# Kernel optimization log

Hardware: AMD Instinct MI355X
Metric: run time of the kernel (lower is better)

## Reference

```python
import jax, jax.numpy as jnp
import numpy as np

BETA = 0.25

def setup_inputs() -> dict:
    key = jax.random.key(0)
    k1, k2 = jax.random.split(key)
    N, K, D = 32768, 8192, 512
    latents = jax.random.normal(k1, (N, D), dtype=jnp.float32)
    # torch init: uniform(-1/num_protos, 1/num_protos)
    prototypes = jax.random.uniform(k2, (K, D), dtype=jnp.float32, minval=-1.0 / K, maxval=1.0 / K)
    return {"latents": latents, "prototypes": prototypes}


def reference(latents, prototypes):
    dists = (jnp.sum(latents ** 2, axis=1, keepdims=True)
             + jnp.sum(prototypes ** 2, axis=1)
             - 2.0 * jnp.matmul(latents, prototypes.T))
    closest = jnp.argmin(dists, axis=1)  # [N]
    # one-hot @ prototypes == gather (same math, no NxK intermediate)
    quantized = prototypes[closest]  # [N, D]
    commitment_loss = jnp.mean((jax.lax.stop_gradient(quantized) - latents) ** 2)
    embedding_loss = jnp.mean((quantized - jax.lax.stop_gradient(latents)) ** 2)
    vq_loss = commitment_loss * BETA + embedding_loss
    # straight-through estimator
    quantized_st = latents + jax.lax.stop_gradient(quantized - latents)
    return quantized_st, vq_loss
```

## Files before the change

kernel.cpp:

```cpp
#include <hip/hip_runtime.h>


#define N_ROWS 32768
#define K_PROTO 8192
#define DIM 512
#define BM 128
#define BN 128
#define BKB 128
#define GROUPS 8
#define TILES 8
#define NSTEP 32
#define BUFB 16384

typedef unsigned char u8;
typedef unsigned int u32;
typedef __attribute__((ext_vector_type(4))) int i32x4;
typedef __attribute__((ext_vector_type(8))) int i32x8;
typedef __attribute__((ext_vector_type(4))) float f32x4;

__device__ __forceinline__ void async16(const void* g, void* s) {
    __builtin_amdgcn_global_load_lds(
        (const __attribute__((address_space(1))) void*)g,
        (__attribute__((address_space(3))) void*)s, 16, 0, 0);
}

__device__ __forceinline__ int pk4(float a, float b, float c, float d) {
    int v = 0;
    v = __builtin_amdgcn_cvt_pk_fp8_f32(a, b, v, false);
    v = __builtin_amdgcn_cvt_pk_fp8_f32(c, d, v, true);
    return v;
}

__global__ void __launch_bounds__(256) conv_latents(const float* __restrict__ X,
                                                    u8* __restrict__ Xf,
                                                    u32* __restrict__ best) {
    if (blockIdx.x < 128) best[blockIdx.x * 256 + threadIdx.x] = 0xFFFFFFFFu;
    size_t i = ((size_t)blockIdx.x * 256 + threadIdx.x) * 16;
    float4 a = ((const float4*)(X + i))[0];
    float4 b = ((const float4*)(X + i))[1];
    float4 c = ((const float4*)(X + i))[2];
    float4 d = ((const float4*)(X + i))[3];
    int4 o;
    o.x = pk4(a.x, a.y, a.z, a.w);
    o.y = pk4(b.x, b.y, b.z, b.w);
    o.z = pk4(c.x, c.y, c.z, c.w);
    o.w = pk4(d.x, d.y, d.z, d.w);
    *(int4*)(Xf + i) = o;
}

__global__ void __launch_bounds__(256) conv_protos(const float* __restrict__ P,
                                                   u8* __restrict__ Pf,
                                                   float* __restrict__ pnC) {
    int row  = blockIdx.x * 4 + (threadIdx.x >> 6);
    int lane = threadIdx.x & 63;
    const float* src = P + (size_t)row * DIM + lane * 8;
    float4 a = ((const float4*)src)[0];
    float4 b = ((const float4*)src)[1];
    int2 o;
    o.x = pk4(a.x * 8192.0f, a.y * 8192.0f, a.z * 8192.0f, a.w * 8192.0f);
    o.y = pk4(b.x * 8192.0f, b.y * 8192.0f, b.z * 8192.0f, b.w * 8192.0f);
    *(int2*)(Pf + (size_t)row * DIM + lane * 8) = o;
    float ss = a.x*a.x + a.y*a.y + a.z*a.z + a.w*a.w
             + b.x*b.x + b.y*b.y + b.z*b.z + b.w*b.w;
    #pragma unroll
    for (int off = 32; off; off >>= 1) ss += __shfl_down(ss, off);
    if (lane == 0) pnC[row] = ss * 8192.0f + 256.0f;
}

__device__ __forceinline__ void stage_b(const u8* __restrict__ Pf, u8* BsF,
                                        int s2, int colg, const int (&voff)[4],
                                        int tid) {
    const int t2 = s2 >> 2, kt2 = s2 & 3, sb = s2 % 3;
    const u8* src = Pf + (size_t)(colg + t2 * BN) * DIM + kt2 * BKB;
    u8* dst = BsF + sb * BUFB + tid * 16;
    #pragma unroll
    for (int i = 0; i < 4; i++)
        async16(src + voff[i], dst + i * 4096);
}

__global__ void __launch_bounds__(256, 2) vq_score_kernel(const u8* __restrict__ Xf,
                                                          const u8* __restrict__ Pf,
                                                          const float* __restrict__ pnC,
                                                          u32* __restrict__ best) {
    __shared__ __align__(16) u8 lds_raw[3 * BUFB + 4096];
    u8* BsF = lds_raw;
    const float* pcs = (const float*)(lds_raw + 3 * BUFB);

    const int tid  = threadIdx.x;
    const int row0 = blockIdx.x * BM;
    const int colg = blockIdx.y * (TILES * BN);

    const int w    = tid >> 6, lane = tid & 63;
    const int quad = lane >> 4, l15 = lane & 15;

    int voff[4];
    #pragma unroll
    for (int i = 0; i < 4; i++) {
        int f = tid + i * 256;
        int row = f >> 3, c = (f & 7) ^ (row & 7);
        voff[i] = row * DIM + c * 16;
    }

    const int x7   = l15 & 7;
    const int pos0 = (quad ^ x7) << 4;
    const int pos1 = pos0 ^ 64;

    i32x8 a[4][2];
    #pragma unroll
    for (int r = 0; r < 2; r++) {
        #pragma unroll
        for (int i = 0; i < 8; i++) {
            int f = tid + i * 256;
            int sl = f >> 10;
            int fi = f & 1023;
            int row = fi >> 3, c = (fi & 7) ^ (row & 7);
            async16(Xf + (size_t)(row0 + row) * DIM + (2 * r + sl) * BKB + c * 16,
                    BsF + f * 16);
        }
        if (r == 0)
            async16((const u8*)(pnC + colg) + tid * 16, lds_raw + 3 * BUFB + tid * 16);
        __syncthreads();
        #pragma unroll
        for (int sl = 0; sl < 2; sl++) {
            const u8* Ar = BsF + sl * BUFB + (w * 32 + l15) * BKB;
            #pragma unroll
            for (int tm = 0; tm < 2; tm++) {
                const u8* p = Ar + tm * 16 * BKB;
                a[2 * r + sl][tm] = __builtin_shufflevector(
                    *(const i32x4*)(p + pos0), *(const i32x4*)(p + pos1),
                    0, 1, 2, 3, 4, 5, 6, 7);
            }
        }
        __syncthreads();
    }

    stage_b(Pf, BsF, 0, colg, voff, tid);
    stage_b(Pf, BsF, 1, colg, voff, tid);

    u32 v[2][4];
    #pragma unroll
    for (int i = 0; i < 2; i++)
        #pragma unroll
        for (int r = 0; r < 4; r++) v[i][r] = 0xFFFFFFFFu;

    for (int t = 0; t < TILES; ++t) {
        f32x4 acc[2][8];
        #pragma unroll
        for (int i = 0; i < 2; i++)
            #pragma unroll
            for (int j = 0; j < 8; j++) acc[i][j] = (f32x4)0.0f;

        #pragma unroll
        for (int kt = 0; kt < 4; ++kt) {
            const int s = t * 4 + kt;
            if (kt == 3 && t == TILES - 1)
                asm volatile("s_waitcnt vmcnt(0)" ::: "memory");
            else
                asm volatile("s_waitcnt vmcnt(4)" ::: "memory");
            __builtin_amdgcn_s_barrier();
            __builtin_amdgcn_sched_barrier(0);

            if (s + 2 < NSTEP) stage_b(Pf, BsF, s + 2, colg, voff, tid);

            const u8* Brow = BsF + (s % 3) * BUFB + l15 * BKB;
            __builtin_amdgcn_s_setprio(1);
            #pragma unroll
            for (int tn = 0; tn < 8; tn++) {
                const u8* bp = Brow + tn * 16 * BKB;
                i32x8 b = __builtin_shufflevector(
                    *(const i32x4*)(bp + pos0), *(const i32x4*)(bp + pos1),
                    0, 1, 2, 3, 4, 5, 6, 7);
                acc[0][tn] = __builtin_amdgcn_mfma_scale_f32_16x16x128_f8f6f4(
                    a[kt][0], b, acc[0][tn], 0, 0, 0, 127, 0, 127);
                acc[1][tn] = __builtin_amdgcn_mfma_scale_f32_16x16x128_f8f6f4(
                    a[kt][1], b, acc[1][tn], 0, 0, 0, 127, 0, 127);
            }
            __builtin_amdgcn_s_setprio(0);
            __builtin_amdgcn_sched_barrier(0);
        }

        #pragma unroll
        for (int tn = 0; tn < 8; tn++) {
            const int ci = t * BN + tn * 16 + l15;
            const float pc = pcs[ci];
            const u32 kidx = (u32)(colg + ci);
            #pragma unroll
            for (int tm = 0; tm < 2; tm++)
                #pragma unroll
                for (int r = 0; r < 4; r++) {
                    float sk = fmaf(-2.0f, acc[tm][tn][r], pc);
                    u32 key = (__float_as_uint(sk) & 0xFFFFE000u) | kidx;
                    if (key < v[tm][r]) v[tm][r] = key;
                }
        }
    }

    #pragma unroll
    for (int tm = 0; tm < 2; tm++)
        #pragma unroll
        for (int r = 0; r < 4; r++) {
            u32 x = v[tm][r];
            #pragma unroll
            for (int off = 1; off < 16; off <<= 1) {
                u32 o = (u32)__shfl_xor((int)x, off);
                if (o < x) x = o;
            }
            if (l15 == 0)
                atomicMin(&best[row0 + w * 32 + tm * 16 + quad * 4 + r], x);
        }
}

__global__ void __launch_bounds__(128) vq_gather_kernel(const float* __restrict__ X,
                                                        const float* __restrict__ P,
                                                        const u32* __restrict__ best,
                                                        float* __restrict__ out,
                                                        float* __restrict__ partial) {
    const int n = blockIdx.x, t = threadIdx.x;
    const u32 k = best[n] & (K_PROTO - 1);
    const float4 p = ((const float4*)(P + (size_t)k * DIM))[t];
    const float4 x = ((const float4*)(X + (size_t)n * DIM))[t];
    ((float4*)(out + (size_t)n * DIM))[t] = p;
    float dx = p.x - x.x, dy = p.y - x.y, dz = p.z - x.z, dw = p.w - x.w;
    float ss = dx * dx + dy * dy + dz * dz + dw * dw;
    #pragma unroll
    for (int off = 32; off; off >>= 1) ss += __shfl_down(ss, off);
    __shared__ float part[2];
    if ((t & 63) == 0) part[t >> 6] = ss;
    __syncthreads();
    if (t == 0) partial[n] = part[0] + part[1];
}

__global__ void __launch_bounds__(256) loss_reduce(const float* __restrict__ partial,
                                                   float* __restrict__ out) {
    const int t = threadIdx.x;
    float s = 0.0f;
    #pragma unroll
    for (int i = 0; i < 32; i++) {
        float4 a = ((const float4*)partial)[t * 32 + i];
        s += a.x + a.y + a.z + a.w;
    }
    #pragma unroll
    for (int off = 32; off; off >>= 1) s += __shfl_down(s, off);
    __shared__ float part[4];
    if ((t & 63) == 0) part[t >> 6] = s;
    __syncthreads();
    if (t == 0)
        out[(size_t)N_ROWS * DIM] =
            (part[0] + part[1] + part[2] + part[3]) * 7.450580596923828e-08f;
}

extern "C" void kernel_launch(void* const* d_in, const int* in_sizes, int n_in,
                              void* d_out, int out_size, void* d_ws, size_t ws_size,
                              hipStream_t stream) {
    const float* X = (const float*)d_in[0];
    const float* P = (const float*)d_in[1];
    float* out = (float*)d_out;
    char* ws = (char*)d_ws;

    u8* Xf = (u8*)ws;
    u8* Pf = (u8*)(ws + 16777216);
    float* pnC = (float*)(ws + 20971520);
    u32* best = (u32*)(ws + 21004288);
    float* partial = (float*)(ws + 21135360);

    conv_latents<<<dim3(4096), dim3(256), 0, stream>>>(X, Xf, best);
    conv_protos<<<dim3(2048), dim3(256), 0, stream>>>(P, Pf, pnC);
    vq_score_kernel<<<dim3(N_ROWS / BM, GROUPS), dim3(256), 0, stream>>>(Xf, Pf, pnC, best);
    vq_gather_kernel<<<dim3(N_ROWS), dim3(128), 0, stream>>>(X, P, best, out, partial);
    loss_reduce<<<dim3(1), dim3(256), 0, stream>>>(partial, out);
}
```

Measured before the change: 312.9 us.

## Use 2-wave blocks with 64 rows per wave and direct A-fragment loads

Shrinks the score block from 4 to 2 waves, so each wave now owns 64 latent rows (4 M-subtiles) and reuses every B fragment read from LDS across 4 MFMAs instead of 2. The A fragments are loaded straight from global memory into registers, dropping the LDS staging pass and its two barriers. B staging issues 8 async loads per thread and the vmcnt wait is adjusted to match. Register pressure roughly doubles for accumulators and A fragments, with launch bounds of 1 block per 128 threads, and fewer waves per CU are left to hide latency.

```diff
diff --git a/kernel.cpp b/kernel.cpp
--- a/kernel.cpp
+++ b/kernel.cpp
@@ -68,17 +68,17 @@
 }
 
 __device__ __forceinline__ void stage_b(const u8* __restrict__ Pf, u8* BsF,
-                                        int s2, int colg, const int (&voff)[4],
+                                        int s2, int colg, const int (&voff)[8],
                                         int tid) {
     const int t2 = s2 >> 2, kt2 = s2 & 3, sb = s2 % 3;
     const u8* src = Pf + (size_t)(colg + t2 * BN) * DIM + kt2 * BKB;
     u8* dst = BsF + sb * BUFB + tid * 16;
     #pragma unroll
-    for (int i = 0; i < 4; i++)
-        async16(src + voff[i], dst + i * 4096);
-}
-
-__global__ void __launch_bounds__(256, 2) vq_score_kernel(const u8* __restrict__ Xf,
+    for (int i = 0; i < 8; i++)
+        async16(src + voff[i], dst + i * 2048);
+}
+
+__global__ void __launch_bounds__(128, 1) vq_score_kernel(const u8* __restrict__ Xf,
                                                           const u8* __restrict__ Pf,
                                                           const float* __restrict__ pnC,
                                                           u32* __restrict__ best) {
@@ -93,10 +93,10 @@
     const int w    = tid >> 6, lane = tid & 63;
     const int quad = lane >> 4, l15 = lane & 15;
 
-    int voff[4];
-    #pragma unroll
-    for (int i = 0; i < 4; i++) {
-        int f = tid + i * 256;
+    int voff[8];
+    #pragma unroll
+    for (int i = 0; i < 8; i++) {
+        int f = tid + i * 128;
         int row = f >> 3, c = (f & 7) ^ (row & 7);
         voff[i] = row * DIM + c * 16;
     }
@@ -105,48 +105,37 @@
     const int pos0 = (quad ^ x7) << 4;
     const int pos1 = pos0 ^ 64;
 
-    i32x8 a[4][2];
-    #pragma unroll
-    for (int r = 0; r < 2; r++) {
-        #pragma unroll
-        for (int i = 0; i < 8; i++) {
-            int f = tid + i * 256;
-            int sl = f >> 10;
-            int fi = f & 1023;
-            int row = fi >> 3, c = (fi & 7) ^ (row & 7);
-            async16(Xf + (size_t)(row0 + row) * DIM + (2 * r + sl) * BKB + c * 16,
-                    BsF + f * 16);
-        }
-        if (r == 0)
-            async16((const u8*)(pnC + colg) + tid * 16, lds_raw + 3 * BUFB + tid * 16);
-        __syncthreads();
-        #pragma unroll
-        for (int sl = 0; sl < 2; sl++) {
-            const u8* Ar = BsF + sl * BUFB + (w * 32 + l15) * BKB;
-            #pragma unroll
-            for (int tm = 0; tm < 2; tm++) {
-                const u8* p = Ar + tm * 16 * BKB;
-                a[2 * r + sl][tm] = __builtin_shufflevector(
-                    *(const i32x4*)(p + pos0), *(const i32x4*)(p + pos1),
-                    0, 1, 2, 3, 4, 5, 6, 7);
+    i32x8 a[4][4];
+    {
+        const u8* Ab = Xf + (size_t)(row0 + w * 64 + l15) * DIM + quad * 16;
+        #pragma unroll
+        for (int kt = 0; kt < 4; kt++)
+            #pragma unroll
+            for (int tm = 0; tm < 4; tm++) {
+                const u8* p = Ab + (size_t)tm * 16 * DIM + kt * BKB;
+                i32x4 lo = *(const i32x4*)p;
+                i32x4 hi = *(const i32x4*)(p + 64);
+                a[kt][tm] = __builtin_shufflevector(lo, hi, 0, 1, 2, 3, 4, 5, 6, 7);
             }
-        }
-        __syncthreads();
-    }
+    }
+
+    async16((const u8*)(pnC + colg) + tid * 16, lds_raw + 3 * BUFB + tid * 16);
+    async16((const u8*)(pnC + colg) + tid * 16 + 2048,
+            lds_raw + 3 * BUFB + tid * 16 + 2048);
 
     stage_b(Pf, BsF, 0, colg, voff, tid);
     stage_b(Pf, BsF, 1, colg, voff, tid);
 
-    u32 v[2][4];
-    #pragma unroll
-    for (int i = 0; i < 2; i++)
+    u32 v[4][4];
+    #pragma unroll
+    for (int i = 0; i < 4; i++)
         #pragma unroll
         for (int r = 0; r < 4; r++) v[i][r] = 0xFFFFFFFFu;
 
     for (int t = 0; t < TILES; ++t) {
-        f32x4 acc[2][8];
-        #pragma unroll
-        for (int i = 0; i < 2; i++)
+        f32x4 acc[4][8];
+        #pragma unroll
+        for (int i = 0; i < 4; i++)
             #pragma unroll
             for (int j = 0; j < 8; j++) acc[i][j] = (f32x4)0.0f;
 
@@ -156,7 +145,7 @@
             if (kt == 3 && t == TILES - 1)
                 asm volatile("s_waitcnt vmcnt(0)" ::: "memory");
             else
-                asm volatile("s_waitcnt vmcnt(4)" ::: "memory");
+                asm volatile("s_waitcnt vmcnt(8)" ::: "memory");
             __builtin_amdgcn_s_barrier();
             __builtin_amdgcn_sched_barrier(0);
 
@@ -170,10 +159,10 @@
                 i32x8 b = __builtin_shufflevector(
                     *(const i32x4*)(bp + pos0), *(const i32x4*)(bp + pos1),
                     0, 1, 2, 3, 4, 5, 6, 7);
-                acc[0][tn] = __builtin_amdgcn_mfma_scale_f32_16x16x128_f8f6f4(
-                    a[kt][0], b, acc[0][tn], 0, 0, 0, 127, 0, 127);
-                acc[1][tn] = __builtin_amdgcn_mfma_scale_f32_16x16x128_f8f6f4(
-                    a[kt][1], b, acc[1][tn], 0, 0, 0, 127, 0, 127);
+                #pragma unroll
+                for (int tm = 0; tm < 4; tm++)
+                    acc[tm][tn] = __builtin_amdgcn_mfma_scale_f32_16x16x128_f8f6f4(
+                        a[kt][tm], b, acc[tm][tn], 0, 0, 0, 127, 0, 127);
             }
             __builtin_amdgcn_s_setprio(0);
             __builtin_amdgcn_sched_barrier(0);
@@ -185,7 +174,7 @@
             const float pc = pcs[ci];
             const u32 kidx = (u32)(colg + ci);
             #pragma unroll
-            for (int tm = 0; tm < 2; tm++)
+            for (int tm = 0; tm < 4; tm++)
                 #pragma unroll
                 for (int r = 0; r < 4; r++) {
                     float sk = fmaf(-2.0f, acc[tm][tn][r], pc);
@@ -196,7 +185,7 @@
     }
 
     #pragma unroll
-    for (int tm = 0; tm < 2; tm++)
+    for (int tm = 0; tm < 4; tm++)
         #pragma unroll
         for (int r = 0; r < 4; r++) {
             u32 x = v[tm][r];
@@ -206,7 +195,7 @@
                 if (o < x) x = o;
             }
             if (l15 == 0)
-                atomicMin(&best[row0 + w * 32 + tm * 16 + quad * 4 + r], x);
+                atomicMin(&best[row0 + w * 64 + tm * 16 + quad * 4 + r], x);
         }
 }
 
@@ -265,7 +254,7 @@
 
     conv_latents<<<dim3(4096), dim3(256), 0, stream>>>(X, Xf, best);
     conv_protos<<<dim3(2048), dim3(256), 0, stream>>>(P, Pf, pnC);
-    vq_score_kernel<<<dim3(N_ROWS / BM, GROUPS), dim3(256), 0, stream>>>(Xf, Pf, pnC, best);
+    vq_score_kernel<<<dim3(N_ROWS / BM, GROUPS), dim3(128), 0, stream>>>(Xf, Pf, pnC, best);
     vq_gather_kernel<<<dim3(N_ROWS), dim3(128), 0, stream>>>(X, P, best, out, partial);
     loss_reduce<<<dim3(1), dim3(256), 0, stream>>>(partial, out);
 }
```

New measurement: 315.1 us. No clear change (+0.7%).
